# Performance work log

Hardware: AMD Instinct MI355X
Metric: run time of the kernel (lower is better)

## Reference

```python
import jax, jax.numpy as jnp
import numpy as np

N_HEADS = 8
N_LSTM_LAYERS = 32
HID = 25  # LSTM hidden units == decoder seq_len
EPS = 1e-5


def _layernorm(x, g, b):
    m = x.mean(-1, keepdims=True)
    v = x.var(-1, keepdims=True)  # biased, as torch LayerNorm
    return (x - m) / jnp.sqrt(v + EPS) * g + b


def _mha(q_in, k_in, v_in, Wq, bq, Wk, bk, Wv, bv, Wo, bo):
    B, L, D = q_in.shape
    S = k_in.shape[1]
    E = D // N_HEADS
    q = (q_in @ Wq + bq).reshape(B, L, N_HEADS, E)
    k = (k_in @ Wk + bk).reshape(B, S, N_HEADS, E)
    v = (v_in @ Wv + bv).reshape(B, S, N_HEADS, E)
    scores = jnp.einsum('blhe,bshe->bhls', q, k) / jnp.sqrt(jnp.asarray(E, q.dtype))
    attn = jax.nn.softmax(scores, axis=-1)
    out = jnp.einsum('bhls,bshe->blhe', attn, v).reshape(B, L, D)
    return out @ Wo + bo


def _lstm_layer(inp, W_ih, W_hh, b_ih, b_hh):
    # inp: [B, T, F]; PyTorch gate order i, f, g, o
    B = inp.shape[0]
    h0 = jnp.zeros((B, HID), inp.dtype)
    c0 = jnp.zeros((B, HID), inp.dtype)
    bias = b_ih + b_hh

    def step(carry, x_t):
        h, c = carry
        gates = x_t @ W_ih.T + h @ W_hh.T + bias  # [B, 4H]
        i, f, g, o = jnp.split(gates, 4, axis=-1)
        c = jax.nn.sigmoid(f) * c + jax.nn.sigmoid(i) * jnp.tanh(g)
        h = jax.nn.sigmoid(o) * jnp.tanh(c)
        return (h, c), h

    xs = jnp.swapaxes(inp, 0, 1)  # [T, B, F]
    _, hs = jax.lax.scan(step, (h0, c0), xs)
    return jnp.swapaxes(hs, 0, 1)  # [B, T, H]


def _forward(x, cross,
             Wq_s, bq_s, Wk_s, bk_s, Wv_s, bv_s, Wo_s, bo_s,
             Wq_c, bq_c, Wk_c, bk_c, Wv_c, bv_c, Wo_c, bo_c,
             g1, b1, g2, b2, g3, b3,
             W_ih, W_hh, b_ih, b_hh, Wc, bc):
    x = x + _mha(x, x, x, Wq_s, bq_s, Wk_s, bk_s, Wv_s, bv_s, Wo_s, bo_s)
    x = _layernorm(x, g1, b1)
    x = x + _mha(x, cross, cross, Wq_c, bq_c, Wk_c, bk_c, Wv_c, bv_c, Wo_c, bo_c)
    x = _layernorm(x, g2, b2)
    # LSTM runs over the feature axis: [B, L=25, D=512] -> [B, T=512, F=25]
    y = jnp.swapaxes(x, 1, 2)
    for l in range(N_LSTM_LAYERS):
        y = _lstm_layer(y, W_ih[l], W_hh[l], b_ih[l], b_hh[l])
    # pointwise conv over channels (dim 1 of [B, 512, 25])
    final_y = jnp.einsum('oc,bcl->bol', Wc, y) + bc[None, :, None]
    final_y = jnp.swapaxes(final_y, 1, 2)  # [B, 25, 512]
    return _layernorm(x + final_y, g3, b3)


def setup_inputs() -> dict:
    key = jax.random.key(0)
    ks = jax.random.split(key, 24)
    B, L, S, D = 128, 25, 96, 512

    def rn(k, shape, scale=0.02):
        return jax.random.normal(k, shape, jnp.float32) * scale

    inp = {
        'x': jax.random.normal(ks[0], (B, L, D), jnp.float32),
        'cross': jax.random.normal(ks[1], (B, S, D), jnp.float32),
        'Wq_s': rn(ks[2], (D, D)), 'bq_s': jnp.zeros(D),
        'Wk_s': rn(ks[3], (D, D)), 'bk_s': jnp.zeros(D),
        'Wv_s': rn(ks[4], (D, D)), 'bv_s': jnp.zeros(D),
        'Wo_s': rn(ks[5], (D, D)), 'bo_s': jnp.zeros(D),
        'Wq_c': rn(ks[6], (D, D)), 'bq_c': jnp.zeros(D),
        'Wk_c': rn(ks[7], (D, D)), 'bk_c': jnp.zeros(D),
        'Wv_c': rn(ks[8], (D, D)), 'bv_c': jnp.zeros(D),
        'Wo_c': rn(ks[9], (D, D)), 'bo_c': jnp.zeros(D),
        'g1': jnp.ones(D), 'b1': jnp.zeros(D),
        'g2': jnp.ones(D), 'b2': jnp.zeros(D),
        'g3': jnp.ones(D), 'b3': jnp.zeros(D),
        'W_ih': rn(ks[10], (N_LSTM_LAYERS, 4 * HID, HID), 0.1),
        'W_hh': rn(ks[11], (N_LSTM_LAYERS, 4 * HID, HID), 0.1),
        'b_ih': jnp.zeros((N_LSTM_LAYERS, 4 * HID)),
        'b_hh': jnp.zeros((N_LSTM_LAYERS, 4 * HID)),
        'Wc': rn(ks[12], (D, D)), 'bc': jnp.zeros(D),
    }
    return inp


def reference(x, cross,
              Wq_s, bq_s, Wk_s, bk_s, Wv_s, bv_s, Wo_s, bo_s,
              Wq_c, bq_c, Wk_c, bk_c, Wv_c, bv_c, Wo_c, bo_c,
              g1, b1, g2, b2, g3, b3,
              W_ih, W_hh, b_ih, b_hh, Wc, bc):
    return _forward(x, cross,
                    Wq_s, bq_s, Wk_s, bk_s, Wv_s, bv_s, Wo_s, bo_s,
                    Wq_c, bq_c, Wk_c, bk_c, Wv_c, bv_c, Wo_c, bo_c,
                    g1, b1, g2, b2, g3, b3,
                    W_ih, W_hh, b_ih, b_hh, Wc, bc)
```

## Files before the change

kernel.cpp:

```cpp
#include <hip/hip_runtime.h>


#define EPS_LN 1e-5f

typedef _Float16 h2v __attribute__((ext_vector_type(2)));
typedef _Float16 h8v __attribute__((ext_vector_type(8)));
typedef float    f4v __attribute__((ext_vector_type(4)));

#if defined(__has_builtin)
#if __has_builtin(__builtin_amdgcn_fdot2)
#define HAVE_FDOT2 1
#endif
#endif

__device__ __forceinline__ float fdot2(h2v a, h2v b, float c) {
#ifdef HAVE_FDOT2
  return __builtin_amdgcn_fdot2(a, b, c, false);
#else
  return c + (float)a.x * (float)b.x + (float)a.y * (float)b.y;
#endif
}
__device__ __forceinline__ h2v bch2(unsigned int u) {
  return __builtin_bit_cast(h2v, u);
}

struct WPtrs { const float* p[9]; };

__global__ __launch_bounds__(256)
void prep_weights(WPtrs w, _Float16* __restrict__ dst) {
  __shared__ float tile[32][33];
  const int z = blockIdx.z;
  const int tx = threadIdx.x & 31, ty = threadIdx.x >> 5;
  const int bx = blockIdx.x, by = blockIdx.y;
  const float* in = w.p[z];
  _Float16* outp = dst + (size_t)z * 262144;
  if (z < 8) {
#pragma unroll
    for (int i = 0; i < 4; i++)
      tile[ty + i * 8][tx] = in[(size_t)(by * 32 + ty + i * 8) * 512 + bx * 32 + tx];
    __syncthreads();
#pragma unroll
    for (int i = 0; i < 4; i++)
      outp[(size_t)(bx * 32 + ty + i * 8) * 512 + by * 32 + tx] = (_Float16)tile[tx][ty + i * 8];
  } else {
#pragma unroll
    for (int i = 0; i < 4; i++) {
      size_t off = (size_t)(by * 32 + ty + i * 8) * 512 + bx * 32 + tx;
      outp[off] = (_Float16)in[off];
    }
  }
}

__global__ __launch_bounds__(256)
void gemm3(const float* __restrict__ A,
           const _Float16* __restrict__ BT0, const _Float16* __restrict__ BT1,
           const _Float16* __restrict__ BT2,
           const float* __restrict__ bias0, const float* __restrict__ bias1,
           const float* __restrict__ bias2,
           float* __restrict__ C0, float* __restrict__ C1, float* __restrict__ C2,
           int M) {
  __shared__ _Float16 Asld[64 * 40];
  __shared__ _Float16 Bsld[64 * 40];
  const int t = threadIdx.x;
  const int which = blockIdx.x >> 3;
  const int n0 = (blockIdx.x & 7) * 64;
  const int m0 = blockIdx.y * 64;
  const _Float16* BT = (which == 0) ? BT0 : (which == 1) ? BT1 : BT2;
  const float* bias  = (which == 0) ? bias0 : (which == 1) ? bias1 : bias2;
  float* C           = (which == 0) ? C0 : (which == 1) ? C1 : C2;

  const int r = t >> 2, q = t & 3;
  const int w = t >> 6;
  const int lane = t & 63;
  const int lm = lane & 15, q8 = lane >> 4;

  f4v acc[4] = {};
  for (int k0 = 0; k0 < 512; k0 += 32) {
    __syncthreads();
    float4 f0 = *(const float4*)&A[(size_t)(m0 + r) * 512 + k0 + q * 8];
    float4 f1 = *(const float4*)&A[(size_t)(m0 + r) * 512 + k0 + q * 8 + 4];
    h8v hvv = {(_Float16)f0.x, (_Float16)f0.y, (_Float16)f0.z, (_Float16)f0.w,
               (_Float16)f1.x, (_Float16)f1.y, (_Float16)f1.z, (_Float16)f1.w};
    *(h8v*)&Asld[r * 40 + q * 8] = hvv;
    *(uint4*)&Bsld[r * 40 + q * 8] = *(const uint4*)&BT[(size_t)(n0 + r) * 512 + k0 + q * 8];
    __syncthreads();
    h8v a = *(const h8v*)&Asld[(w * 16 + lm) * 40 + q8 * 8];
#pragma unroll
    for (int nt = 0; nt < 4; nt++) {
      h8v b = *(const h8v*)&Bsld[(nt * 16 + lm) * 40 + q8 * 8];
      acc[nt] = __builtin_amdgcn_mfma_f32_16x16x32_f16(a, b, acc[nt], 0, 0, 0);
    }
  }
#pragma unroll
  for (int nt = 0; nt < 4; nt++) {
    int gn = n0 + nt * 16 + lm;
    float bv = bias[gn];
#pragma unroll
    for (int rg = 0; rg < 4; rg++) {
      int gm = m0 + w * 16 + q8 * 4 + rg;
      C[(size_t)gm * 512 + gn] = acc[nt][rg] + bv;
    }
  }
}

template <int S>
__global__ __launch_bounds__(256)
void attn_scores(const float* __restrict__ Q, const float* __restrict__ K,
                 float* __restrict__ P) {
  __shared__ float Qs[25][64];
  __shared__ float Ks[S][65];
  const int h = blockIdx.x, b = blockIdx.y, t = threadIdx.x;
  for (int idx = t; idx < 25 * 64; idx += 256) {
    int l = idx >> 6, e = idx & 63;
    Qs[l][e] = Q[(b * 25 + l) * 512 + h * 64 + e];
  }
  for (int idx = t; idx < S * 64; idx += 256) {
    int s = idx >> 6, e = idx & 63;
    Ks[s][e] = K[(b * S + s) * 512 + h * 64 + e];
  }
  __syncthreads();
  float* Pb = P + (size_t)(b * 8 + h) * 25 * S;
  for (int idx = t; idx < 25 * S; idx += 256) {
    int l = idx / S, s = idx % S;
    float acc = 0.f;
#pragma unroll
    for (int e = 0; e < 64; e++) acc += Qs[l][e] * Ks[s][e];
    Pb[idx] = acc * 0.125f;
  }
}

template <int S>
__global__ __launch_bounds__(256)
void attn_out(const float* __restrict__ P, const float* __restrict__ V,
              float* __restrict__ O) {
  __shared__ float Ps[25][S];
  __shared__ float Vs[S][64];
  const int h = blockIdx.x, b = blockIdx.y, t = threadIdx.x;
  const float* Pb = P + (size_t)(b * 8 + h) * 25 * S;
  for (int idx = t; idx < 25 * S; idx += 256) Ps[idx / S][idx % S] = Pb[idx];
  for (int idx = t; idx < S * 64; idx += 256) {
    int s = idx >> 6, e = idx & 63;
    Vs[s][e] = V[(b * S + s) * 512 + h * 64 + e];
  }
  __syncthreads();
  if (t < 25) {
    float mx = -1e30f;
    for (int s = 0; s < S; s++) mx = fmaxf(mx, Ps[t][s]);
    float sum = 0.f;
    for (int s = 0; s < S; s++) { float p = __expf(Ps[t][s] - mx); Ps[t][s] = p; sum += p; }
    float r = 1.f / sum;
    for (int s = 0; s < S; s++) Ps[t][s] *= r;
  }
  __syncthreads();
  for (int idx = t; idx < 25 * 64; idx += 256) {
    int l = idx >> 6, e = idx & 63;
    float acc = 0.f;
    for (int s = 0; s < S; s++) acc += Ps[l][s] * Vs[s][e];
    O[(b * 25 + l) * 512 + h * 64 + e] = acc;
  }
}

__global__ __launch_bounds__(128)
void add_ln(const float* __restrict__ a, const float* __restrict__ b,
            const float* __restrict__ gw, const float* __restrict__ bw,
            float* __restrict__ out) {
  const int row = blockIdx.x, t = threadIdx.x;
  float4 va = ((const float4*)(a + (size_t)row * 512))[t];
  float4 vb = ((const float4*)(b + (size_t)row * 512))[t];
  float4 v = make_float4(va.x + vb.x, va.y + vb.y, va.z + vb.z, va.w + vb.w);
  float s = v.x + v.y + v.z + v.w;
  float q = v.x * v.x + v.y * v.y + v.z * v.z + v.w * v.w;
#pragma unroll
  for (int off = 32; off > 0; off >>= 1) {
    s += __shfl_down(s, off);
    q += __shfl_down(q, off);
  }
  __shared__ float red[4];
  if ((t & 63) == 0) { red[(t >> 6) * 2] = s; red[(t >> 6) * 2 + 1] = q; }
  __syncthreads();
  float S_ = red[0] + red[2], Q_ = red[1] + red[3];
  float mean = S_ * (1.f / 512.f);
  float var  = Q_ * (1.f / 512.f) - mean * mean;
  float inv  = rsqrtf(var + EPS_LN);
  float4 g4 = ((const float4*)gw)[t];
  float4 b4 = ((const float4*)bw)[t];
  float4 o;
  o.x = (v.x - mean) * inv * g4.x + b4.x;
  o.y = (v.y - mean) * inv * g4.y + b4.y;
  o.z = (v.z - mean) * inv * g4.z + b4.z;
  o.w = (v.w - mean) * inv * g4.w + b4.w;
  ((float4*)(out + (size_t)row * 512))[t] = o;
}

__global__ void transpose_dl(const float* __restrict__ in, float* __restrict__ outp) {
  const int b = blockIdx.x, t = threadIdx.x;
  for (int idx = t; idx < 25 * 512; idx += 256) {
    int l2 = idx / 512, c = idx % 512;
    outp[((size_t)b * 25 + l2) * 512 + c] = in[((size_t)b * 512 + c) * 25 + l2];
  }
}

__global__ __launch_bounds__(256)
void prep_x0r(const float* __restrict__ x2, _Float16* __restrict__ X0) {
  __shared__ float tile[25][516];
  const int b = blockIdx.x, t = threadIdx.x;
  for (int idx = t; idx < 25 * 512; idx += 256) {
    int u = idx >> 9, d = idx & 511;
    tile[u][d] = x2[((size_t)b * 25 + u) * 512 + d];
  }
  __syncthreads();
  for (int idx = t; idx < 512 * 32; idx += 256) {
    int d = idx >> 5, u = idx & 31;
    X0[((size_t)b * 512 + d) * 32 + u] = (u < 25) ? (_Float16)tile[u][d] : (_Float16)0.f;
  }
}

#define NLAY 32
#define NGRP 32
#define BGRP 4
#define CHT  8
#define NCHK 64
#define RSLOTS 64
#define RCHK (RSLOTS / CHT)
#define RLAY ((size_t)128 * RSLOTS * 32)

__device__ __forceinline__ int ld_rlx(int* p) {
  return __hip_atomic_load(p, __ATOMIC_RELAXED, __HIP_MEMORY_SCOPE_AGENT);
}
__device__ __forceinline__ void st_rlx(int* p, int v) {
  __hip_atomic_store(p, v, __ATOMIC_RELAXED, __HIP_MEMORY_SCOPE_AGENT);
}
__device__ __forceinline__ unsigned long long ldq_rlx(const unsigned long long* p) {
  return __hip_atomic_load(p, __ATOMIC_RELAXED, __HIP_MEMORY_SCOPE_AGENT);
}
__device__ __forceinline__ void sth_rlx(_Float16* p, _Float16 v) {
  __hip_atomic_store((unsigned short*)p, __builtin_bit_cast(unsigned short, v),
                     __ATOMIC_RELAXED, __HIP_MEMORY_SCOPE_AGENT);
}
__device__ __forceinline__ float tanh_fast(float x) {
  return 1.f - 2.f / (1.f + __expf(2.f * x));
}

__global__ __launch_bounds__(256) __attribute__((amdgpu_waves_per_eu(4, 4)))
void lstm_pipeline(const _Float16* __restrict__ X0, float* __restrict__ yout,
                   _Float16* __restrict__ ring, int* __restrict__ prod,
                   int* __restrict__ cons,
                   const float* __restrict__ Wih, const float* __restrict__ Whh,
                   const float* __restrict__ bih, const float* __restrict__ bhh) {
  const int l = blockIdx.x / NGRP;
  const int g = blockIdx.x % NGRP;
  const int t = threadIdx.x;
  const int lane = t & 63;
  const int wv   = t >> 6;
  const bool gate_lane = (lane < 50);
  const bool unit_lane = (lane < 25);

  __shared__ _Float16 xbuf[CHT][BGRP][32];
  __shared__ _Float16 hbuf[BGRP][32];

  h2v wih2[2][13], whh2[2][13];
  float bias_r[2];
  float c_reg = 0.f;
  {
    const int r0 = gate_lane ? lane : 49;
#pragma unroll
    for (int j = 0; j < 2; j++) {
      const int row = r0 + j * 50;
      const float* wi = &Wih[((size_t)l * 100 + row) * 25];
      const float* wh = &Whh[((size_t)l * 100 + row) * 25];
#pragma unroll
      for (int k = 0; k < 13; k++) {
        float alo = wi[2 * k], ahi = (2 * k + 1 < 25) ? wi[2 * k + 1] : 0.f;
        float blo = wh[2 * k], bhi = (2 * k + 1 < 25) ? wh[2 * k + 1] : 0.f;
        wih2[j][k] = h2v{(_Float16)alo, (_Float16)ahi};
        whh2[j][k] = h2v{(_Float16)blo, (_Float16)bhi};
      }
      bias_r[j] = bih[l * 100 + row] + bhh[l * 100 + row];
    }
  }
  for (int idx = t; idx < BGRP * 32; idx += 256) (&hbuf[0][0])[idx] = (_Float16)0.f;
  __syncthreads();

  const int bglob = g * BGRP + wv;
  _Float16* ring_out = ring + (size_t)l * RLAY
                       + ((size_t)bglob * RSLOTS) * 32 + lane;
  float* yout_out = yout + ((size_t)bglob * 512) * 25 + lane;

  const int s_tc = t >> 5, s_b2 = (t >> 3) & 3, s_seg = t & 7;

  int* prod_in   = prod + (l - 1) * NGRP + g;
  int* prod_out  = prod + l * NGRP + g;
  int* cons_self = cons + l * NGRP + g;
  int* cons_up   = cons + (l + 1) * NGRP + g;

  for (int n = 0; n < NCHK; n++) {
    if (t == 0) {
      if (l > 0) {
        while (ld_rlx(prod_in) < n + 1) __builtin_amdgcn_s_sleep(1);
      }
      if (l < NLAY - 1 && n >= RCHK) {
        while (ld_rlx(cons_up) < n - RCHK + 1) __builtin_amdgcn_s_sleep(1);
      }
    }
    __syncthreads();
    {
      const int tg = n * CHT + s_tc;
      if (l == 0) {
        unsigned long long a = *(const unsigned long long*)(X0
            + (((size_t)(g * BGRP + s_b2) * 512) + tg) * 32 + s_seg * 4);
        *(unsigned long long*)&xbuf[s_tc][s_b2][s_seg * 4] = a;
      } else {
        const unsigned long long* p = (const unsigned long long*)(ring
            + (size_t)(l - 1) * RLAY
            + (((size_t)(g * BGRP + s_b2) * RSLOTS) + (tg & (RSLOTS - 1))) * 32
            + s_seg * 4);
        unsigned long long a = ldq_rlx(p);
        *(unsigned long long*)&xbuf[s_tc][s_b2][s_seg * 4] = a;
      }
    }
    __syncthreads();
    if (t == 0 && l > 0) st_rlx(cons_self, n + 1);

    float ax[CHT][2];
    if (gate_lane) {
#pragma unroll
      for (int tc = 0; tc < CHT; tc++) {
        const unsigned int* xr = (const unsigned int*)&xbuf[tc][wv][0];
        uint4 xa = *(const uint4*)(xr);
        uint4 xb = *(const uint4*)(xr + 4);
        uint4 xc = *(const uint4*)(xr + 8);
        unsigned int xd = xr[12];
        h2v xk[13] = {bch2(xa.x), bch2(xa.y), bch2(xa.z), bch2(xa.w),
                      bch2(xb.x), bch2(xb.y), bch2(xb.z), bch2(xb.w),
                      bch2(xc.x), bch2(xc.y), bch2(xc.z), bch2(xc.w),
                      bch2(xd)};
        float a0 = bias_r[0], a1 = bias_r[1];
#pragma unroll
        for (int k = 0; k < 13; k++) {
          a0 = fdot2(wih2[0][k], xk[k], a0);
          a1 = fdot2(wih2[1][k], xk[k], a1);
        }
        ax[tc][0] = a0; ax[tc][1] = a1;
      }
    }

#pragma unroll
    for (int tc = 0; tc < CHT; tc++) {
      const int tg = n * CHT + tc;
      float s0 = 0.f, sg1 = 0.f, th1 = 0.f;
      if (gate_lane) {
        const unsigned int* hr = (const unsigned int*)&hbuf[wv][0];
        uint4 ha = *(const uint4*)(hr);
        uint4 hb = *(const uint4*)(hr + 4);
        uint4 hc = *(const uint4*)(hr + 8);
        unsigned int hd = hr[12];
        h2v hk[13] = {bch2(ha.x), bch2(ha.y), bch2(ha.z), bch2(ha.w),
                      bch2(hb.x), bch2(hb.y), bch2(hb.z), bch2(hb.w),
                      bch2(hc.x), bch2(hc.y), bch2(hc.z), bch2(hc.w),
                      bch2(hd)};
        float a0 = ax[tc][0], a1 = ax[tc][1];
#pragma unroll
        for (int k = 0; k < 13; k++) {
          a0 = fdot2(whh2[0][k], hk[k], a0);
          a1 = fdot2(whh2[1][k], hk[k], a1);
        }
        s0  = 1.f / (1.f + __expf(-a0));
        sg1 = 1.f / (1.f + __expf(-a1));
        th1 = tanh_fast(a1);
      }
      float sf = __shfl(s0,  lane + 25);
      float so = __shfl(sg1, lane + 25);
      if (unit_lane) {
        c_reg = sf * c_reg + s0 * th1;
        float h = so * tanh_fast(c_reg);
        _Float16 h16 = (_Float16)h;
        hbuf[wv][lane] = h16;
        if (l == NLAY - 1)
          yout_out[(size_t)tg * 25] = h;
        else
          sth_rlx(ring_out + (size_t)(tg & (RSLOTS - 1)) * 32, h16);
      }
    }
    asm volatile("s_waitcnt vmcnt(0)" ::: "memory");
    __syncthreads();
    if (t == 0 && l < NLAY - 1) st_rlx(prod_out, n + 1);
  }
}

extern "C" void kernel_launch(void* const* d_in, const int* in_sizes, int n_in,
                              void* d_out, int out_size, void* d_ws, size_t ws_size,
                              hipStream_t stream) {
  const float* x     = (const float*)d_in[0];
  const float* cross = (const float*)d_in[1];
  const float* Wq_s = (const float*)d_in[2];  const float* bq_s = (const float*)d_in[3];
  const float* Wk_s = (const float*)d_in[4];  const float* bk_s = (const float*)d_in[5];
  const float* Wv_s = (const float*)d_in[6];  const float* bv_s = (const float*)d_in[7];
  const float* Wo_s = (const float*)d_in[8];  const float* bo_s = (const float*)d_in[9];
  const float* Wq_c = (const float*)d_in[10]; const float* bq_c = (const float*)d_in[11];
  const float* Wk_c = (const float*)d_in[12]; const float* bk_c = (const float*)d_in[13];
  const float* Wv_c = (const float*)d_in[14]; const float* bv_c = (const float*)d_in[15];
  const float* Wo_c = (const float*)d_in[16]; const float* bo_c = (const float*)d_in[17];
  const float* g1 = (const float*)d_in[18]; const float* b1 = (const float*)d_in[19];
  const float* g2 = (const float*)d_in[20]; const float* b2 = (const float*)d_in[21];
  const float* g3 = (const float*)d_in[22]; const float* b3 = (const float*)d_in[23];
  const float* Wih = (const float*)d_in[24];
  const float* Whh = (const float*)d_in[25];
  const float* bih = (const float*)d_in[26];
  const float* bhh = (const float*)d_in[27];
  const float* Wc  = (const float*)d_in[28]; const float* bc = (const float*)d_in[29];
  float* out = (float*)d_out;
  float* ws  = (float*)d_ws;

  constexpr size_t A  = 1638400;
  constexpr size_t C6 = 6291456;
  float* x1    = ws;
  float* Qc    = ws + A;
  float* Qs    = ws + 2 * A;
  float* Ks    = ws + 3 * A;
  float* Vs    = ws + 4 * A;
  float* attns = ws + 5 * A;
  float* tmp   = ws + 6 * A;
  float* Ps    = ws + 7 * A;
  float* Kc    = ws + 2 * A;
  float* Vc    = ws + 2 * A + C6;
  float* attnc = ws + 2 * A + 2 * C6;
  float* Pc    = attnc + A;
  float* tmp2  = ws + 6 * A;
  float* x2    = ws + 3 * A;
  _Float16* X0b  = (_Float16*)(ws + 4 * A);
  float*    youtb = ws + 5 * A;
  _Float16* ringb = (_Float16*)(ws + 6 * A);
  float* ytb   = ws + 2 * A;
  float* fy    = ws + 5 * A;
  _Float16* WTall = (_Float16*)(ws + 20000000);
  int* ctr = (int*)(ws + 21179648);

  dim3 blk(256);
  WPtrs wpq;
  wpq.p[0] = Wq_s; wpq.p[1] = Wk_s; wpq.p[2] = Wv_s; wpq.p[3] = Wo_s;
  wpq.p[4] = Wq_c; wpq.p[5] = Wk_c; wpq.p[6] = Wv_c; wpq.p[7] = Wo_c;
  wpq.p[8] = Wc;
  prep_weights<<<dim3(16, 16, 9), blk, 0, stream>>>(wpq, WTall);
  hipMemsetAsync(ctr, 0, 2048 * sizeof(int), stream);
  _Float16* WT[9];
  for (int i = 0; i < 9; i++) WT[i] = WTall + (size_t)i * 262144;

  gemm3<<<dim3(24, 50), blk, 0, stream>>>(x, WT[0], WT[1], WT[2],
                                          bq_s, bk_s, bv_s, Qs, Ks, Vs, 3200);
  attn_scores<25><<<dim3(8, 128), blk, 0, stream>>>(Qs, Ks, Ps);
  attn_out<25><<<dim3(8, 128), blk, 0, stream>>>(Ps, Vs, attns);
  gemm3<<<dim3(8, 50), blk, 0, stream>>>(attns, WT[3], WT[3], WT[3],
                                         bo_s, bo_s, bo_s, tmp, tmp, tmp, 3200);
  add_ln<<<3200, 128, 0, stream>>>(x, tmp, g1, b1, x1);
  gemm3<<<dim3(8, 50), blk, 0, stream>>>(x1, WT[4], WT[4], WT[4],
                                         bq_c, bq_c, bq_c, Qc, Qc, Qc, 3200);
  gemm3<<<dim3(16, 192), blk, 0, stream>>>(cross, WT[5], WT[6], WT[6],
                                           bk_c, bv_c, bv_c, Kc, Vc, Vc, 12288);
  attn_scores<96><<<dim3(8, 128), blk, 0, stream>>>(Qc, Kc, Pc);
  attn_out<96><<<dim3(8, 128), blk, 0, stream>>>(Pc, Vc, attnc);
  gemm3<<<dim3(8, 50), blk, 0, stream>>>(attnc, WT[7], WT[7], WT[7],
                                         bo_c, bo_c, bo_c, tmp2, tmp2, tmp2, 3200);
  add_ln<<<3200, 128, 0, stream>>>(x1, tmp2, g2, b2, x2);
  prep_x0r<<<128, 256, 0, stream>>>(x2, X0b);
  lstm_pipeline<<<NLAY * NGRP, 256, 0, stream>>>(X0b, youtb, ringb, ctr, ctr + 1024,
                                                 Wih, Whh, bih, bhh);
  transpose_dl<<<128, 256, 0, stream>>>(youtb, ytb);
  gemm3<<<dim3(8, 50), blk, 0, stream>>>(ytb, WT[8], WT[8], WT[8],
                                         bc, bc, bc, fy, fy, fy, 3200);
  add_ln<<<3200, 128, 0, stream>>>(x2, fy, g3, b3, out);
}
```

Before: 1.048 ms.

## Process two batch rows per wave in LSTM pipeline, halving block count

Each wave in the layer-pipelined LSTM now handles two batch rows instead of one, so each block covers 8 batches and there are 16 groups per layer instead of 32. The recurrent weights held in registers are reused across both rows, and the two independent dependency chains can hide each other's latency. The per-block loads of the input chunk are widened, and the counter arrays are resized to match. Sigmoid and tanh now use a hardware reciprocal instead of a divide. The trade-off is more registers per wave (occupancy hint lowered to 2 waves/EU) and fewer blocks in the grid.

```diff
diff --git a/kernel.cpp b/kernel.cpp
--- a/kernel.cpp
+++ b/kernel.cpp
@@ -10,6 +10,9 @@
 #if defined(__has_builtin)
 #if __has_builtin(__builtin_amdgcn_fdot2)
 #define HAVE_FDOT2 1
+#endif
+#if __has_builtin(__builtin_amdgcn_rcpf)
+#define HAVE_RCPF 1
 #endif
 #endif
 
@@ -22,6 +25,19 @@
 }
 __device__ __forceinline__ h2v bch2(unsigned int u) {
   return __builtin_bit_cast(h2v, u);
+}
+__device__ __forceinline__ float rcp_fast(float x) {
+#ifdef HAVE_RCPF
+  return __builtin_amdgcn_rcpf(x);
+#else
+  return 1.f / x;
+#endif
+}
+__device__ __forceinline__ float sigm_fast(float x) {
+  return rcp_fast(1.f + __expf(-x));
+}
+__device__ __forceinline__ float tanh_fast(float x) {
+  return 1.f - 2.f * rcp_fast(1.f + __expf(2.f * x));
 }
 
 struct WPtrs { const float* p[9]; };
@@ -216,8 +232,8 @@
 }
 
 #define NLAY 32
-#define NGRP 32
-#define BGRP 4
+#define NGRP 16
+#define BGRP 8
 #define CHT  8
 #define NCHK 64
 #define RSLOTS 64
@@ -237,11 +253,8 @@
   __hip_atomic_store((unsigned short*)p, __builtin_bit_cast(unsigned short, v),
                      __ATOMIC_RELAXED, __HIP_MEMORY_SCOPE_AGENT);
 }
-__device__ __forceinline__ float tanh_fast(float x) {
-  return 1.f - 2.f / (1.f + __expf(2.f * x));
-}
-
-__global__ __launch_bounds__(256) __attribute__((amdgpu_waves_per_eu(4, 4)))
+
+__global__ __launch_bounds__(256) __attribute__((amdgpu_waves_per_eu(2, 2)))
 void lstm_pipeline(const _Float16* __restrict__ X0, float* __restrict__ yout,
                    _Float16* __restrict__ ring, int* __restrict__ prod,
                    int* __restrict__ cons,
@@ -252,17 +265,17 @@
   const int t = threadIdx.x;
   const int lane = t & 63;
   const int wv   = t >> 6;
-  const bool gate_lane = (lane < 50);
-  const bool unit_lane = (lane < 25);
+  const int bA   = wv * 2;
+  const int bB   = wv * 2 + 1;
 
   __shared__ _Float16 xbuf[CHT][BGRP][32];
   __shared__ _Float16 hbuf[BGRP][32];
 
   h2v wih2[2][13], whh2[2][13];
   float bias_r[2];
-  float c_reg = 0.f;
+  float cA = 0.f, cB = 0.f;
   {
-    const int r0 = gate_lane ? lane : 49;
+    const int r0 = (lane < 50) ? lane : 49;
 #pragma unroll
     for (int j = 0; j < 2; j++) {
       const int row = r0 + j * 50;
@@ -281,12 +294,13 @@
   for (int idx = t; idx < BGRP * 32; idx += 256) (&hbuf[0][0])[idx] = (_Float16)0.f;
   __syncthreads();
 
-  const int bglob = g * BGRP + wv;
-  _Float16* ring_out = ring + (size_t)l * RLAY
-                       + ((size_t)bglob * RSLOTS) * 32 + lane;
-  float* yout_out = yout + ((size_t)bglob * 512) * 25 + lane;
-
-  const int s_tc = t >> 5, s_b2 = (t >> 3) & 3, s_seg = t & 7;
+  const int gbA = g * BGRP + bA, gbB = g * BGRP + bB;
+  _Float16* ring_outA = ring + (size_t)l * RLAY + ((size_t)gbA * RSLOTS) * 32 + lane;
+  _Float16* ring_outB = ring + (size_t)l * RLAY + ((size_t)gbB * RSLOTS) * 32 + lane;
+  float* yout_outA = yout + ((size_t)gbA * 512) * 25 + lane;
+  float* yout_outB = yout + ((size_t)gbB * 512) * 25 + lane;
+
+  const int s_tc = t >> 5, s_b2 = (t >> 2) & 7, s_seg = t & 3;
 
   int* prod_in   = prod + (l - 1) * NGRP + g;
   int* prod_out  = prod + l * NGRP + g;
@@ -306,79 +320,116 @@
     {
       const int tg = n * CHT + s_tc;
       if (l == 0) {
-        unsigned long long a = *(const unsigned long long*)(X0
-            + (((size_t)(g * BGRP + s_b2) * 512) + tg) * 32 + s_seg * 4);
-        *(unsigned long long*)&xbuf[s_tc][s_b2][s_seg * 4] = a;
+        const uint4* p = (const uint4*)(X0
+            + (((size_t)(g * BGRP + s_b2) * 512) + tg) * 32 + s_seg * 8);
+        *(uint4*)&xbuf[s_tc][s_b2][s_seg * 8] = *p;
       } else {
         const unsigned long long* p = (const unsigned long long*)(ring
             + (size_t)(l - 1) * RLAY
             + (((size_t)(g * BGRP + s_b2) * RSLOTS) + (tg & (RSLOTS - 1))) * 32
-            + s_seg * 4);
+            + s_seg * 8);
         unsigned long long a = ldq_rlx(p);
-        *(unsigned long long*)&xbuf[s_tc][s_b2][s_seg * 4] = a;
+        unsigned long long b = ldq_rlx(p + 1);
+        *(uint4*)&xbuf[s_tc][s_b2][s_seg * 8] =
+            make_uint4((unsigned)a, (unsigned)(a >> 32),
+                       (unsigned)b, (unsigned)(b >> 32));
       }
     }
     __syncthreads();
     if (t == 0 && l > 0) st_rlx(cons_self, n + 1);
 
-    float ax[CHT][2];
-    if (gate_lane) {
-#pragma unroll
-      for (int tc = 0; tc < CHT; tc++) {
-        const unsigned int* xr = (const unsigned int*)&xbuf[tc][wv][0];
-        uint4 xa = *(const uint4*)(xr);
-        uint4 xb = *(const uint4*)(xr + 4);
-        uint4 xc = *(const uint4*)(xr + 8);
-        unsigned int xd = xr[12];
-        h2v xk[13] = {bch2(xa.x), bch2(xa.y), bch2(xa.z), bch2(xa.w),
-                      bch2(xb.x), bch2(xb.y), bch2(xb.z), bch2(xb.w),
-                      bch2(xc.x), bch2(xc.y), bch2(xc.z), bch2(xc.w),
-                      bch2(xd)};
-        float a0 = bias_r[0], a1 = bias_r[1];
-#pragma unroll
-        for (int k = 0; k < 13; k++) {
-          a0 = fdot2(wih2[0][k], xk[k], a0);
-          a1 = fdot2(wih2[1][k], xk[k], a1);
-        }
-        ax[tc][0] = a0; ax[tc][1] = a1;
-      }
+    float axA[CHT][2], axB[CHT][2];
+#pragma unroll
+    for (int tc = 0; tc < CHT; tc++) {
+      const unsigned int* xrA = (const unsigned int*)&xbuf[tc][bA][0];
+      const unsigned int* xrB = (const unsigned int*)&xbuf[tc][bB][0];
+      uint4 xaA = *(const uint4*)(xrA);
+      uint4 xbA = *(const uint4*)(xrA + 4);
+      uint4 xcA = *(const uint4*)(xrA + 8);
+      unsigned int xdA = xrA[12];
+      uint4 xaB = *(const uint4*)(xrB);
+      uint4 xbB = *(const uint4*)(xrB + 4);
+      uint4 xcB = *(const uint4*)(xrB + 8);
+      unsigned int xdB = xrB[12];
+      h2v xkA[13] = {bch2(xaA.x), bch2(xaA.y), bch2(xaA.z), bch2(xaA.w),
+                     bch2(xbA.x), bch2(xbA.y), bch2(xbA.z), bch2(xbA.w),
+                     bch2(xcA.x), bch2(xcA.y), bch2(xcA.z), bch2(xcA.w),
+                     bch2(xdA)};
+      h2v xkB[13] = {bch2(xaB.x), bch2(xaB.y), bch2(xaB.z), bch2(xaB.w),
+                     bch2(xbB.x), bch2(xbB.y), bch2(xbB.z), bch2(xbB.w),
+                     bch2(xcB.x), bch2(xcB.y), bch2(xcB.z), bch2(xcB.w),
+                     bch2(xdB)};
+      float a0A = bias_r[0], a1A = bias_r[1];
+      float a0B = bias_r[0], a1B = bias_r[1];
+#pragma unroll
+      for (int k = 0; k < 13; k++) {
+        a0A = fdot2(wih2[0][k], xkA[k], a0A);
+        a1A = fdot2(wih2[1][k], xkA[k], a1A);
+        a0B = fdot2(wih2[0][k], xkB[k], a0B);
+        a1B = fdot2(wih2[1][k], xkB[k], a1B);
+      }
+      axA[tc][0] = a0A; axA[tc][1] = a1A;
+      axB[tc][0] = a0B; axB[tc][1] = a1B;
     }
 
 #pragma unroll
     for (int tc = 0; tc < CHT; tc++) {
       const int tg = n * CHT + tc;
-      float s0 = 0.f, sg1 = 0.f, th1 = 0.f;
-      if (gate_lane) {
-        const unsigned int* hr = (const unsigned int*)&hbuf[wv][0];
-        uint4 ha = *(const uint4*)(hr);
-        uint4 hb = *(const uint4*)(hr + 4);
-        uint4 hc = *(const uint4*)(hr + 8);
-        unsigned int hd = hr[12];
-        h2v hk[13] = {bch2(ha.x), bch2(ha.y), bch2(ha.z), bch2(ha.w),
-                      bch2(hb.x), bch2(hb.y), bch2(hb.z), bch2(hb.w),
-                      bch2(hc.x), bch2(hc.y), bch2(hc.z), bch2(hc.w),
-                      bch2(hd)};
-        float a0 = ax[tc][0], a1 = ax[tc][1];
-#pragma unroll
-        for (int k = 0; k < 13; k++) {
-          a0 = fdot2(whh2[0][k], hk[k], a0);
-          a1 = fdot2(whh2[1][k], hk[k], a1);
+      const unsigned int* hrA = (const unsigned int*)&hbuf[bA][0];
+      uint4 haA = *(const uint4*)(hrA);
+      uint4 hbA_ = *(const uint4*)(hrA + 4);
+      uint4 hcA = *(const uint4*)(hrA + 8);
+      unsigned int hdA = hrA[12];
+      h2v hkA[13] = {bch2(haA.x), bch2(haA.y), bch2(haA.z), bch2(haA.w),
+                     bch2(hbA_.x), bch2(hbA_.y), bch2(hbA_.z), bch2(hbA_.w),
+                     bch2(hcA.x), bch2(hcA.y), bch2(hcA.z), bch2(hcA.w),
+                     bch2(hdA)};
+      float a0A = axA[tc][0], a1A = axA[tc][1];
+      const unsigned int* hrB = (const unsigned int*)&hbuf[bB][0];
+      uint4 haB = *(const uint4*)(hrB);
+      uint4 hbB_ = *(const uint4*)(hrB + 4);
+      uint4 hcB = *(const uint4*)(hrB + 8);
+      unsigned int hdB = hrB[12];
+      h2v hkB[13] = {bch2(haB.x), bch2(haB.y), bch2(haB.z), bch2(haB.w),
+                     bch2(hbB_.x), bch2(hbB_.y), bch2(hbB_.z), bch2(hbB_.w),
+                     bch2(hcB.x), bch2(hcB.y), bch2(hcB.z), bch2(hcB.w),
+                     bch2(hdB)};
+      float a0B = axB[tc][0], a1B = axB[tc][1];
+#pragma unroll
+      for (int k = 0; k < 13; k++) {
+        a0A = fdot2(whh2[0][k], hkA[k], a0A);
+        a1A = fdot2(whh2[1][k], hkA[k], a1A);
+        a0B = fdot2(whh2[0][k], hkB[k], a0B);
+        a1B = fdot2(whh2[1][k], hkB[k], a1B);
+      }
+      float s0A  = sigm_fast(a0A);
+      float sg1A = sigm_fast(a1A);
+      float th1A = tanh_fast(a1A);
+      float s0B  = sigm_fast(a0B);
+      float sg1B = sigm_fast(a1B);
+      float th1B = tanh_fast(a1B);
+      float sfA = __shfl(s0A,  lane + 25);
+      float soA = __shfl(sg1A, lane + 25);
+      float sfB = __shfl(s0B,  lane + 25);
+      float soB = __shfl(sg1B, lane + 25);
+      cA = sfA * cA + s0A * th1A;
+      cB = sfB * cB + s0B * th1B;
+      float hA = soA * tanh_fast(cA);
+      float hB = soB * tanh_fast(cB);
+      _Float16 hA16 = (_Float16)hA;
+      _Float16 hB16 = (_Float16)hB;
+      if (lane < 32) {
+        hbuf[bA][lane] = hA16;
+        hbuf[bB][lane] = hB16;
+      }
+      if (lane < 25) {
+        if (l == NLAY - 1) {
+          yout_outA[(size_t)tg * 25] = hA;
+          yout_outB[(size_t)tg * 25] = hB;
+        } else {
+          sth_rlx(ring_outA + (size_t)(tg & (RSLOTS - 1)) * 32, hA16);
+          sth_rlx(ring_outB + (size_t)(tg & (RSLOTS - 1)) * 32, hB16);
         }
-        s0  = 1.f / (1.f + __expf(-a0));
-        sg1 = 1.f / (1.f + __expf(-a1));
-        th1 = tanh_fast(a1);
-      }
-      float sf = __shfl(s0,  lane + 25);
-      float so = __shfl(sg1, lane + 25);
-      if (unit_lane) {
-        c_reg = sf * c_reg + s0 * th1;
-        float h = so * tanh_fast(c_reg);
-        _Float16 h16 = (_Float16)h;
-        hbuf[wv][lane] = h16;
-        if (l == NLAY - 1)
-          yout_out[(size_t)tg * 25] = h;
-        else
-          sth_rlx(ring_out + (size_t)(tg & (RSLOTS - 1)) * 32, h16);
       }
     }
     asm volatile("s_waitcnt vmcnt(0)" ::: "memory");
@@ -441,7 +492,7 @@
   wpq.p[4] = Wq_c; wpq.p[5] = Wk_c; wpq.p[6] = Wv_c; wpq.p[7] = Wo_c;
   wpq.p[8] = Wc;
   prep_weights<<<dim3(16, 16, 9), blk, 0, stream>>>(wpq, WTall);
-  hipMemsetAsync(ctr, 0, 2048 * sizeof(int), stream);
+  hipMemsetAsync(ctr, 0, 1024 * sizeof(int), stream);
   _Float16* WT[9];
   for (int i = 0; i < 9; i++) WT[i] = WTall + (size_t)i * 262144;
 
@@ -462,7 +513,7 @@
                                          bo_c, bo_c, bo_c, tmp2, tmp2, tmp2, 3200);
   add_ln<<<3200, 128, 0, stream>>>(x1, tmp2, g2, b2, x2);
   prep_x0r<<<128, 256, 0, stream>>>(x2, X0b);
-  lstm_pipeline<<<NLAY * NGRP, 256, 0, stream>>>(X0b, youtb, ringb, ctr, ctr + 1024,
+  lstm_pipeline<<<NLAY * NGRP, 256, 0, stream>>>(X0b, youtb, ringb, ctr, ctr + 512,
                                                  Wih, Whh, bih, bhh);
   transpose_dl<<<128, 256, 0, stream>>>(youtb, ytb);
   gemm3<<<dim3(8, 50), blk, 0, stream>>>(ytb, WT[8], WT[8], WT[8],
```

Measured after the change: 1.397 ms. 1.33x slower.

## Broadcast LSTM hidden state via readlane instead of LDS and rebalance gate lanes

Applied to the files above, without the earlier changes.

Reorganizes the per-wave LSTM recurrence so the two 32-lane halves each compute paired gates (i/g and f/o) and exchange them with a single xor shuffle. The new hidden state is broadcast to registers with readlane instead of a write and read through shared memory, which removes an LDS round trip from the serial per-timestep critical path. It also replaces the divisions in sigmoid and tanh with a hardware reciprocal. The costs are 25 scalar readlanes per step, duplicated work on the padding lanes, and slightly lower precision from the approximate reciprocal.

```diff
diff --git a/kernel.cpp b/kernel.cpp
--- a/kernel.cpp
+++ b/kernel.cpp
@@ -10,6 +10,9 @@
 #if defined(__has_builtin)
 #if __has_builtin(__builtin_amdgcn_fdot2)
 #define HAVE_FDOT2 1
+#endif
+#if __has_builtin(__builtin_amdgcn_rcpf)
+#define HAVE_RCPF 1
 #endif
 #endif
 
@@ -22,6 +25,19 @@
 }
 __device__ __forceinline__ h2v bch2(unsigned int u) {
   return __builtin_bit_cast(h2v, u);
+}
+__device__ __forceinline__ float rcp_fast(float x) {
+#ifdef HAVE_RCPF
+  return __builtin_amdgcn_rcpf(x);
+#else
+  return 1.f / x;
+#endif
+}
+__device__ __forceinline__ float sigm_fast(float x) {
+  return rcp_fast(1.f + __expf(-x));
+}
+__device__ __forceinline__ float tanh_fast(float x) {
+  return 1.f - 2.f * rcp_fast(1.f + __expf(2.f * x));
 }
 
 struct WPtrs { const float* p[9]; };
@@ -237,9 +253,6 @@
   __hip_atomic_store((unsigned short*)p, __builtin_bit_cast(unsigned short, v),
                      __ATOMIC_RELAXED, __HIP_MEMORY_SCOPE_AGENT);
 }
-__device__ __forceinline__ float tanh_fast(float x) {
-  return 1.f - 2.f / (1.f + __expf(2.f * x));
-}
 
 __global__ __launch_bounds__(256) __attribute__((amdgpu_waves_per_eu(4, 4)))
 void lstm_pipeline(const _Float16* __restrict__ X0, float* __restrict__ yout,
@@ -252,17 +265,19 @@
   const int t = threadIdx.x;
   const int lane = t & 63;
   const int wv   = t >> 6;
-  const bool gate_lane = (lane < 50);
-  const bool unit_lane = (lane < 25);
+  const bool lo  = (lane < 32);
 
   __shared__ _Float16 xbuf[CHT][BGRP][32];
-  __shared__ _Float16 hbuf[BGRP][32];
 
   h2v wih2[2][13], whh2[2][13];
   float bias_r[2];
   float c_reg = 0.f;
+  h2v hk[13];
+#pragma unroll
+  for (int k = 0; k < 13; k++) hk[k] = h2v{(_Float16)0.f, (_Float16)0.f};
   {
-    const int r0 = gate_lane ? lane : 49;
+    const int uu = ((lane & 31) < 25) ? (lane & 31) : 24;
+    const int r0 = uu + (lane >> 5) * 25;
 #pragma unroll
     for (int j = 0; j < 2; j++) {
       const int row = r0 + j * 50;
@@ -278,7 +293,6 @@
       bias_r[j] = bih[l * 100 + row] + bhh[l * 100 + row];
     }
   }
-  for (int idx = t; idx < BGRP * 32; idx += 256) (&hbuf[0][0])[idx] = (_Float16)0.f;
   __syncthreads();
 
   const int bglob = g * BGRP + wv;
@@ -322,63 +336,60 @@
     if (t == 0 && l > 0) st_rlx(cons_self, n + 1);
 
     float ax[CHT][2];
-    if (gate_lane) {
-#pragma unroll
-      for (int tc = 0; tc < CHT; tc++) {
-        const unsigned int* xr = (const unsigned int*)&xbuf[tc][wv][0];
-        uint4 xa = *(const uint4*)(xr);
-        uint4 xb = *(const uint4*)(xr + 4);
-        uint4 xc = *(const uint4*)(xr + 8);
-        unsigned int xd = xr[12];
-        h2v xk[13] = {bch2(xa.x), bch2(xa.y), bch2(xa.z), bch2(xa.w),
-                      bch2(xb.x), bch2(xb.y), bch2(xb.z), bch2(xb.w),
-                      bch2(xc.x), bch2(xc.y), bch2(xc.z), bch2(xc.w),
-                      bch2(xd)};
-        float a0 = bias_r[0], a1 = bias_r[1];
-#pragma unroll
-        for (int k = 0; k < 13; k++) {
-          a0 = fdot2(wih2[0][k], xk[k], a0);
-          a1 = fdot2(wih2[1][k], xk[k], a1);
-        }
-        ax[tc][0] = a0; ax[tc][1] = a1;
-      }
+#pragma unroll
+    for (int tc = 0; tc < CHT; tc++) {
+      const unsigned int* xr = (const unsigned int*)&xbuf[tc][wv][0];
+      uint4 xa = *(const uint4*)(xr);
+      uint4 xb = *(const uint4*)(xr + 4);
+      uint4 xc = *(const uint4*)(xr + 8);
+      unsigned int xd = xr[12];
+      h2v xk[13] = {bch2(xa.x), bch2(xa.y), bch2(xa.z), bch2(xa.w),
+                    bch2(xb.x), bch2(xb.y), bch2(xb.z), bch2(xb.w),
+                    bch2(xc.x), bch2(xc.y), bch2(xc.z), bch2(xc.w),
+                    bch2(xd)};
+      float a0 = bias_r[0], a1 = bias_r[1];
+#pragma unroll
+      for (int k = 0; k < 13; k++) {
+        a0 = fdot2(wih2[0][k], xk[k], a0);
+        a1 = fdot2(wih2[1][k], xk[k], a1);
+      }
+      ax[tc][0] = a0; ax[tc][1] = a1;
     }
 
 #pragma unroll
     for (int tc = 0; tc < CHT; tc++) {
       const int tg = n * CHT + tc;
-      float s0 = 0.f, sg1 = 0.f, th1 = 0.f;
-      if (gate_lane) {
-        const unsigned int* hr = (const unsigned int*)&hbuf[wv][0];
-        uint4 ha = *(const uint4*)(hr);
-        uint4 hb = *(const uint4*)(hr + 4);
-        uint4 hc = *(const uint4*)(hr + 8);
-        unsigned int hd = hr[12];
-        h2v hk[13] = {bch2(ha.x), bch2(ha.y), bch2(ha.z), bch2(ha.w),
-                      bch2(hb.x), bch2(hb.y), bch2(hb.z), bch2(hb.w),
-                      bch2(hc.x), bch2(hc.y), bch2(hc.z), bch2(hc.w),
-                      bch2(hd)};
-        float a0 = ax[tc][0], a1 = ax[tc][1];
-#pragma unroll
-        for (int k = 0; k < 13; k++) {
-          a0 = fdot2(whh2[0][k], hk[k], a0);
-          a1 = fdot2(whh2[1][k], hk[k], a1);
-        }
-        s0  = 1.f / (1.f + __expf(-a0));
-        sg1 = 1.f / (1.f + __expf(-a1));
-        th1 = tanh_fast(a1);
-      }
-      float sf = __shfl(s0,  lane + 25);
-      float so = __shfl(sg1, lane + 25);
-      if (unit_lane) {
-        c_reg = sf * c_reg + s0 * th1;
-        float h = so * tanh_fast(c_reg);
-        _Float16 h16 = (_Float16)h;
-        hbuf[wv][lane] = h16;
+      float a0 = ax[tc][0], a1 = ax[tc][1];
+#pragma unroll
+      for (int k = 0; k < 13; k++) {
+        a0 = fdot2(whh2[0][k], hk[k], a0);
+        a1 = fdot2(whh2[1][k], hk[k], a1);
+      }
+      float p0 = sigm_fast(a0);
+      float p1 = lo ? tanh_fast(a1) : sigm_fast(a1);
+      float q0 = __shfl_xor(p0, 32, 64);
+      float q1 = __shfl_xor(p1, 32, 64);
+      float si  = lo ? p0 : q0;
+      float sf  = lo ? q0 : p0;
+      float tg_ = lo ? p1 : q1;
+      float so  = lo ? q1 : p1;
+      c_reg = sf * c_reg + si * tg_;
+      float h = so * tanh_fast(c_reg);
+      _Float16 h16 = (_Float16)h;
+      unsigned hu = (unsigned)__builtin_bit_cast(unsigned short, h16);
+      if (lane < 25) {
         if (l == NLAY - 1)
           yout_out[(size_t)tg * 25] = h;
         else
           sth_rlx(ring_out + (size_t)(tg & (RSLOTS - 1)) * 32, h16);
+      }
+#pragma unroll
+      for (int k = 0; k < 13; k++) {
+        unsigned lo16 = ((unsigned)__builtin_amdgcn_readlane((int)hu, 2 * k)) & 0xffffu;
+        unsigned hi16 = (2 * k + 1 < 25)
+            ? (((unsigned)__builtin_amdgcn_readlane((int)hu, 2 * k + 1)) << 16)
+            : 0u;
+        hk[k] = bch2(lo16 | hi16);
       }
     }
     asm volatile("s_waitcnt vmcnt(0)" ::: "memory");
```

New measurement: 3.386 ms. +223.0%, slower.
